# Optimization experiments

Measured on AMD Instinct MI355X. Metric: run time of the kernel, lower is better.

The kernel has to match this reference:

```python
import jax, jax.numpy as jnp
import numpy as np

B, C, H, W = 32, 3, 224, 224
PH = PW = 16
N = (H // PH) * (W // PW)          # 196 patches
PATCH_DIM = C * PH * PW             # 768
DIM = 512
NUM_CLASSES = 1000
LAMBDA = 1.0                        # lambda_=1 in OptimAttn
RHO = 1.0                           # ADMM penalty
ADMM_ITERS = 50                     # fixed iteration count (jit-friendly)
LN_EPS = 1e-5


def layernorm(x, g, b):
    mu = jnp.mean(x, axis=-1, keepdims=True)
    var = jnp.mean((x - mu) ** 2, axis=-1, keepdims=True)
    return (x - mu) / jnp.sqrt(var + LN_EPS) * g + b


def box_qp_admm(Q1, p, iters=ADMM_ITERS, rho=RHO):
    """Solve min_x 0.5 x^T Q1 x + p^T x  s.t. 0 <= x <= 1, batched.
    Q1: [b, m, m] (shared across the n query tokens), p: [b, n, m].
    ADMM splitting x = z; x-update uses the precomputed inverse of (Q1 + rho I).
    Returns z: [b, n, m] (feasible iterate)."""
    b, n, m = p.shape
    Minv = jnp.linalg.inv(Q1 + rho * jnp.eye(m, dtype=Q1.dtype))  # [b, m, m]

    def step(carry, _):
        z, u = carry
        rhs = rho * (z - u) - p                        # [b, n, m]
        x = jnp.einsum('bij,bnj->bni', Minv, rhs)       # [b, n, m]
        z = jnp.clip(x + u, 0.0, 1.0)                   # box projection (lb=0, ub=1)
        u = u + x - z
        return (z, u), None

    z0 = jnp.zeros_like(p)
    u0 = jnp.zeros_like(p)
    (z, _), _ = jax.lax.scan(step, (z0, u0), None, length=iters)
    return z


def setup_inputs() -> dict:
    key = jax.random.key(0)
    ks = jax.random.split(key, 8)
    s = 0.02
    return {
        'img': jax.random.normal(ks[0], (B, C, H, W), jnp.float32),
        'ln_patch_g': jnp.ones((PATCH_DIM,), jnp.float32),
        'ln_patch_b': jnp.zeros((PATCH_DIM,), jnp.float32),
        'wq_w': jax.random.normal(ks[1], (PATCH_DIM, DIM), jnp.float32) * s,
        'wq_b': jnp.zeros((DIM,), jnp.float32),
        'lnq_g': jnp.ones((DIM,), jnp.float32),
        'lnq_b': jnp.zeros((DIM,), jnp.float32),
        'wv_w': jax.random.normal(ks[2], (PATCH_DIM, DIM), jnp.float32) * s,
        'wv_b': jnp.zeros((DIM,), jnp.float32),
        'lnv_g': jnp.ones((DIM,), jnp.float32),
        'lnv_b': jnp.zeros((DIM,), jnp.float32),
        'pos_emb': jax.random.normal(ks[3], (1, N + 1, PATCH_DIM), jnp.float32),
        'mlp_ln_g': jnp.ones((DIM,), jnp.float32),
        'mlp_ln_b': jnp.zeros((DIM,), jnp.float32),
        'mlp_w': jax.random.normal(ks[4], (DIM, NUM_CLASSES), jnp.float32) * s,
        'mlp_b': jnp.zeros((NUM_CLASSES,), jnp.float32),
    }


def reference(img, ln_patch_g, ln_patch_b, wq_w, wq_b, lnq_g, lnq_b,
              wv_w, wv_b, lnv_g, lnv_b, pos_emb, mlp_ln_g, mlp_ln_b,
              mlp_w, mlp_b):
    b = img.shape[0]
    # patchify: b c (h ph) (w pw) -> b (h w) (c ph pw)
    hh, ww = H // PH, W // PW
    x = img.reshape(b, C, hh, PH, ww, PW).transpose(0, 2, 4, 1, 3, 5)
    x = x.reshape(b, hh * ww, PATCH_DIM)
    x = layernorm(x, ln_patch_g, ln_patch_b)
    n = x.shape[1]
    x = x + pos_emb[:, :n]

    Q = layernorm(x @ wq_w + wq_b, lnq_g, lnq_b)   # [b, n, d]
    V = layernorm(x @ wv_w + wv_b, lnv_g, lnv_b)   # [b, m, d]

    # Attention via per-token box QP
    m = V.shape[1]
    V = V / m
    Q1 = 2.0 * jnp.einsum('bmd,bkd->bmk', V, V)                 # [b, m, m]
    p = -2.0 * jnp.einsum('bmd,bnd->bnm', V, Q) + LAMBDA / m    # [b, n, m]
    z = box_qp_admm(Q1, p)                                      # [b, n, m]

    coeffs = z / (jnp.sum(jnp.abs(z), axis=-1, keepdims=True) + 1e-10)
    out = jnp.einsum('bnm,bmd->bnd', coeffs, V)                 # [b, n, d]

    pooled = out.mean(axis=1)                                   # [b, d]
    logits = layernorm(pooled, mlp_ln_g, mlp_ln_b) @ mlp_w + mlp_b
    return jax.nn.softmax(logits, axis=-1)
```

## Files before the change

kernel.cpp:

```cpp
#include <hip/hip_runtime.h>

#define B_ 32
#define NP 196
#define PD 768
#define DM 512
#define NC 1000
#define MAT (NP*NP)

typedef __attribute__((ext_vector_type(8))) short short8;
typedef __attribute__((ext_vector_type(16))) float f32x16;
typedef __attribute__((ext_vector_type(2))) float f32x2;

__device__ inline unsigned short f2bf(float x) {
  union { float f; unsigned u; } c; c.f = x;
  unsigned r = c.u + 0x7FFFu + ((c.u >> 16) & 1u);
  return (unsigned short)(r >> 16);
}
__device__ inline float bf2f(unsigned short h) {
  union { unsigned u; float f; } c; c.u = ((unsigned)h) << 16; return c.f;
}

__device__ inline void pack_store_hi(unsigned short* Bh, int base,
                                     float r0, float r1, float r2, float r3) {
  unsigned short h0=f2bf(r0), h1=f2bf(r1), h2=f2bf(r2), h3=f2bf(r3);
  uint2 vh; vh.x = (unsigned)h0 | ((unsigned)h1<<16); vh.y = (unsigned)h2 | ((unsigned)h3<<16);
  *reinterpret_cast<uint2*>(Bh + base) = vh;
}

__global__ __launch_bounds__(256) void k_patchify(
    const float* __restrict__ img, const float* __restrict__ g,
    const float* __restrict__ be, const float* __restrict__ pos,
    unsigned short* __restrict__ Xh) {
  int bn = blockIdx.x;
  int b = bn / NP, n = bn % NP;
  int gh = n / 14, gw = n % 14;
  int t = threadIdx.x;
  float vals[3]; float s = 0.f, ss = 0.f;
  #pragma unroll
  for (int k = 0; k < 3; ++k) {
    int e = t + (k << 8);
    int inner = e & 255;
    int ph = inner >> 4, pw = inner & 15;
    float v = img[((b*3 + k)*224 + gh*16 + ph)*224 + gw*16 + pw];
    vals[k] = v; s += v; ss += v*v;
  }
  __shared__ float rb[8];
  for (int o = 32; o; o >>= 1) { s += __shfl_down(s,o); ss += __shfl_down(ss,o); }
  if ((t & 63) == 0) { rb[t>>6] = s; rb[4+(t>>6)] = ss; }
  __syncthreads();
  float S = rb[0]+rb[1]+rb[2]+rb[3], SS = rb[4]+rb[5]+rb[6]+rb[7];
  float mu = S * (1.f/768.f);
  float var = SS * (1.f/768.f) - mu*mu;
  float inv = rsqrtf(var + 1e-5f);
  int mt = bn >> 5, ml = bn & 31;
  size_t base = (size_t)mt * 48 * 512;
  #pragma unroll
  for (int k = 0; k < 3; ++k) {
    int e = t + (k << 8);
    float val = (vals[k]-mu)*inv*g[e] + be[e] + pos[n*PD + e];
    int ks = e >> 4, h = (e >> 3) & 1, j = e & 7;
    size_t idx = base + ((size_t)ks*64 + ml + 32*h)*8 + j;
    Xh[idx] = f2bf(val);
  }
}

__global__ __launch_bounds__(256) void k_wswz(
    const float* __restrict__ W,
    unsigned short* __restrict__ Bh) {
  int k = blockIdx.x;
  int t = threadIdx.x;
  int ks = k >> 4, h = (k >> 3) & 1, j = k & 7;
  #pragma unroll
  for (int q = 0; q < 2; ++q) {
    int n = t + (q << 8);
    float v = W[(size_t)k*512 + n];
    size_t idx = (((size_t)(n>>5)*48 + ks)*64 + (n&31) + 32*h)*8 + j;
    Bh[idx] = f2bf(v);
  }
}

__global__ __launch_bounds__(256, 1) void k_qv_mfma(
    const unsigned short* __restrict__ Xh,
    const unsigned short* __restrict__ Wqh,
    const unsigned short* __restrict__ Wvh,
    const float* __restrict__ bq, const float* __restrict__ bv,
    float* __restrict__ qo, float* __restrict__ vo) {
  int bid = blockIdx.x;
  int proj = bid & 1, nq = (bid >> 1) & 3, mp = bid >> 3;
  int mt0 = mp*2, mt1 = mp*2 + 1;
  const unsigned short* Bh = proj ? Wvh : Wqh;
  const float* bias = proj ? bv : bq;
  float* out = proj ? vo : qo;
  int t = threadIdx.x, wv = t >> 6, l = t & 63;
  int n_l = l & 31, h = l >> 5;
  int nt = nq*4 + wv;
  const unsigned short* a0h_p = Xh + (size_t)mt0*48*512 + l*8;
  const unsigned short* a1h_p = Xh + (size_t)mt1*48*512 + l*8;
  const unsigned short* bh_p = Bh + (size_t)nt*48*512 + l*8;
  f32x16 p1_0, p1_1;
  #pragma unroll
  for (int i = 0; i < 16; ++i) { p1_0[i]=0.f; p1_1[i]=0.f; }
  #pragma unroll 4
  for (int ks = 0; ks < 48; ++ks) {
    short8 bh = *reinterpret_cast<const short8*>(bh_p + (size_t)ks*512);
    short8 a0h = *reinterpret_cast<const short8*>(a0h_p + (size_t)ks*512);
    short8 a1h = *reinterpret_cast<const short8*>(a1h_p + (size_t)ks*512);
    p1_0 = __builtin_amdgcn_mfma_f32_32x32x16_bf16(a0h, bh, p1_0, 0, 0, 0);
    p1_1 = __builtin_amdgcn_mfma_f32_32x32x16_bf16(a1h, bh, p1_1, 0, 0, 0);
  }
  float bb = bias[nt*32 + n_l];
  #pragma unroll
  for (int r = 0; r < 16; ++r) {
    int rl = (r&3) + 8*(r>>2) + 4*h;
    out[(size_t)(mt0*32 + rl)*512 + nt*32 + n_l] = p1_0[r] + bb;
    out[(size_t)(mt1*32 + rl)*512 + nt*32 + n_l] = p1_1[r] + bb;
  }
}

__global__ __launch_bounds__(256) void k_ln2(
    const float* __restrict__ q, float* __restrict__ v,
    const float* __restrict__ gq, const float* __restrict__ bq,
    const float* __restrict__ gv, const float* __restrict__ bv,
    unsigned short* __restrict__ Fh) {
  int r = blockIdx.x; bool hv = (r >= B_*NP); if (hv) r -= B_*NP;
  const float* X = hv ? v : q;
  const float* g  = hv ? gv : gq;
  const float* be = hv ? bv : bq;
  float scale = hv ? (1.f/196.f) : 1.f;
  int t = threadIdx.x;
  float v0 = X[(size_t)r*512 + t], v1 = X[(size_t)r*512 + 256 + t];
  float s = v0+v1, ss = v0*v0+v1*v1;
  __shared__ float rb[8];
  for (int o = 32; o; o >>= 1) { s += __shfl_down(s,o); ss += __shfl_down(ss,o); }
  if ((t&63)==0) { rb[t>>6]=s; rb[4+(t>>6)]=ss; }
  __syncthreads();
  float S = rb[0]+rb[1]+rb[2]+rb[3], SS = rb[4]+rb[5]+rb[6]+rb[7];
  float mu = S*(1.f/512.f), var = SS*(1.f/512.f)-mu*mu;
  float inv = rsqrtf(var+1e-5f);
  int b = r / NP, ntok = r % NP;
  int mt = ntok >> 5, ml = ntok & 31;
  size_t fb = (((size_t)b*2 + (hv?1:0))*7 + mt) * 32 * 512;
  float val0 = ((v0-mu)*inv*g[t]+be[t])*scale;
  float val1 = ((v1-mu)*inv*g[t+256]+be[t+256])*scale;
  if (hv) {
    v[(size_t)r*512+t] = val0;
    v[(size_t)r*512+256+t] = val1;
  }
  #pragma unroll
  for (int e2 = 0; e2 < 2; ++e2) {
    int e = t + (e2 << 8);
    float val = e2 ? val1 : val0;
    int ks = e >> 4, h = (e >> 3) & 1, j = e & 7;
    size_t idx = fb + (size_t)ks*512 + ((size_t)ml + 32*h)*8 + j;
    Fh[idx] = f2bf(val);
  }
}

__global__ __launch_bounds__(64) void k_gram_mfma(
    const unsigned short* __restrict__ Fh,
    float* __restrict__ Ao, float* __restrict__ po) {
  int gid = blockIdx.x;
  int mt = gid / 7, nt = gid % 7;
  int z = blockIdx.y; int b = z & 31; bool hp = (z >= 32);
  int l = threadIdx.x;
  int col = l & 31, h2 = l >> 5;
  size_t abase = (((size_t)b*2 + (hp ? 0 : 1))*7 + mt) * 32 * 512 + l*8;
  size_t bbase = (((size_t)b*2 + 1)*7 + nt) * 32 * 512 + l*8;
  f32x16 a1;
  #pragma unroll
  for (int i = 0; i < 16; ++i) { a1[i] = 0.f; }
  #pragma unroll 4
  for (int ks = 0; ks < 32; ++ks) {
    short8 ah = *reinterpret_cast<const short8*>(Fh + abase + (size_t)ks*512);
    short8 bh = *reinterpret_cast<const short8*>(Fh + bbase + (size_t)ks*512);
    a1 = __builtin_amdgcn_mfma_f32_32x32x16_bf16(ah, bh, a1, 0, 0, 0);
  }
  float alpha  = hp ? -2.f : 2.f;
  float diagAdd = hp ? 0.f : 1.f;
  float cAdd   = hp ? (1.f/196.f) : 0.f;
  float* out = (hp ? po : Ao) + (size_t)b*MAT;
  #pragma unroll
  for (int r = 0; r < 16; ++r) {
    int m = mt*32 + (r&3) + 8*(r>>2) + 4*h2;
    int c = nt*32 + col;
    if (m < NP && c < NP)
      out[(size_t)m*NP + c] = alpha*a1[r] + cAdd + (m==c ? diagAdd : 0.f);
  }
}

__global__ __launch_bounds__(256) void k_nsinit2(
    const float* __restrict__ A, float* __restrict__ X, float* __restrict__ Y) {
  int b = blockIdx.x, t = threadIdx.x;
  const float* Ab = A + (size_t)b*MAT;
  __shared__ float sm[256];
  float lm = 0.f;
  if (t < NP) {
    float s = 0.f;
    for (int j = 0; j < NP; ++j) {
      float v = Ab[t*NP + j];
      if (j == t) v -= 1.f;
      s += fabsf(v);
    }
    lm = s;
  }
  sm[t] = lm; __syncthreads();
  for (int o = 128; o; o >>= 1) { if (t < o) sm[t] = fmaxf(sm[t], sm[t+o]); __syncthreads(); }
  float cc = 2.f / (2.f + sm[0]);
  float* Xb = X + (size_t)b*MAT;
  float* Yb = Y + (size_t)b*MAT;
  for (int idx = t; idx < MAT; idx += 256) {
    float yv = cc * Ab[idx];
    Yb[idx] = yv;
    float tpr = cc * yv;
    Xb[idx] = ((idx % (NP+1) == 0) ? 2.f*cc : 0.f) - tpr;
  }
}

__global__ __launch_bounds__(256) void k_ns(
    const float* __restrict__ X, const float* __restrict__ Y,
    float* __restrict__ Xn, float* __restrict__ Yn) {
  int zz = blockIdx.z; int b = zz & 31; bool hy = (zz >= 32);
  const float* Lb = (hy ? Y : X) + (size_t)b*MAT;
  const float* Rb = Y + (size_t)b*MAT;
  float* Ob = (hy ? Yn : Xn) + (size_t)b*MAT;
  int c0 = blockIdx.x * 64, r0 = blockIdx.y * 64;
  __shared__ __align__(16) float Ls[16][68];
  __shared__ __align__(16) float Rs[16][64];
  int t = threadIdx.x, tx = t & 15, ty = t >> 4;
  int alr = t >> 2, alc = (t & 3) << 2;
  int blr = t >> 4, blc = (t & 15) << 2;
  f32x2 acc[4][2];
  #pragma unroll
  for (int i = 0; i < 4; ++i) { acc[i][0] = 0.f; acc[i][1] = 0.f; }
  int lrow = min(r0 + alr, NP-1);
  for (int k0 = 0; k0 < NP; k0 += 16) {
    float4 lv = {0.f,0.f,0.f,0.f};
    if (k0 + alc < NP) lv = *reinterpret_cast<const float4*>(&Lb[(size_t)lrow*NP + k0 + alc]);
    float4 rv = {0.f,0.f,0.f,0.f};
    if (k0 + blr < NP) rv = *reinterpret_cast<const float4*>(&Rb[(size_t)(k0+blr)*NP + c0 + blc]);
    Ls[alc+0][alr] = lv.x; Ls[alc+1][alr] = lv.y;
    Ls[alc+2][alr] = lv.z; Ls[alc+3][alr] = lv.w;
    *reinterpret_cast<float4*>(&Rs[blr][blc]) = rv;
    __syncthreads();
    #pragma unroll
    for (int kt = 0; kt < 16; ++kt) {
      float a4[4];
      *reinterpret_cast<float4*>(a4) = *reinterpret_cast<const float4*>(&Ls[kt][ty<<2]);
      const f32x2* b2 = reinterpret_cast<const f32x2*>(&Rs[kt][tx<<2]);
      f32x2 b20 = b2[0], b21 = b2[1];
      #pragma unroll
      for (int i = 0; i < 4; ++i) {
        f32x2 av; av[0] = a4[i]; av[1] = a4[i];
        acc[i][0] += av * b20;
        acc[i][1] += av * b21;
      }
    }
    __syncthreads();
  }
  #pragma unroll
  for (int i = 0; i < 4; ++i) {
    int r = r0 + (ty<<2) + i; if (r >= NP) continue;
    #pragma unroll
    for (int j = 0; j < 4; ++j) {
      int c = c0 + (tx<<2) + j; if (c >= NP) continue;
      Ob[(size_t)r*NP + c] = 2.f*Lb[(size_t)r*NP + c] - acc[i][j>>1][j&1];
    }
  }
}

__global__ __launch_bounds__(256) void k_ns_last(
    const float* __restrict__ X, const float* __restrict__ Y,
    unsigned short* __restrict__ Ahi) {
  int b = blockIdx.z;
  const float* Lb = X + (size_t)b*MAT;
  const float* Rb = Y + (size_t)b*MAT;
  int c0 = blockIdx.x * 64, r0 = blockIdx.y * 64;
  __shared__ __align__(16) float Ls[16][68];
  __shared__ __align__(16) float Rs[16][64];
  int t = threadIdx.x, tx = t & 15, ty = t >> 4;
  int alr = t >> 2, alc = (t & 3) << 2;
  int blr = t >> 4, blc = (t & 15) << 2;
  f32x2 acc[4][2];
  #pragma unroll
  for (int i = 0; i < 4; ++i) { acc[i][0] = 0.f; acc[i][1] = 0.f; }
  int lrow = min(r0 + alr, NP-1);
  for (int k0 = 0; k0 < NP; k0 += 16) {
    float4 lv = {0.f,0.f,0.f,0.f};
    if (k0 + alc < NP) lv = *reinterpret_cast<const float4*>(&Lb[(size_t)lrow*NP + k0 + alc]);
    float4 rv = {0.f,0.f,0.f,0.f};
    if (k0 + blr < NP) rv = *reinterpret_cast<const float4*>(&Rb[(size_t)(k0+blr)*NP + c0 + blc]);
    Ls[alc+0][alr] = lv.x; Ls[alc+1][alr] = lv.y;
    Ls[alc+2][alr] = lv.z; Ls[alc+3][alr] = lv.w;
    *reinterpret_cast<float4*>(&Rs[blr][blc]) = rv;
    __syncthreads();
    #pragma unroll
    for (int kt = 0; kt < 16; ++kt) {
      float a4[4];
      *reinterpret_cast<float4*>(a4) = *reinterpret_cast<const float4*>(&Ls[kt][ty<<2]);
      const f32x2* b2 = reinterpret_cast<const f32x2*>(&Rs[kt][tx<<2]);
      f32x2 b20 = b2[0], b21 = b2[1];
      #pragma unroll
      for (int i = 0; i < 4; ++i) {
        f32x2 av; av[0] = a4[i]; av[1] = a4[i];
        acc[i][0] += av * b20;
        acc[i][1] += av * b21;
      }
    }
    __syncthreads();
  }
  #pragma unroll
  for (int i = 0; i < 4; ++i) {
    int r = r0 + (ty<<2) + i; if (r >= NP) continue;
    #pragma unroll
    for (int j = 0; j < 4; ++j) {
      int c = c0 + (tx<<2) + j; if (c >= NP) continue;
      float val = 2.f*Lb[(size_t)r*NP + c] - acc[i][j>>1][j&1];
      size_t idx = (((size_t)(b*7 + (r>>5))*13) + (c>>4))*512
                 + (size_t)((r&31) + 32*((c>>3)&1))*8 + (c&7);
      Ahi[idx] = f2bf(val);
    }
  }
}

__global__ __launch_bounds__(448) void k_admm7(
    const unsigned short* __restrict__ Ahi,
    const float* __restrict__ P, float* __restrict__ w) {
  int bid = blockIdx.x;
  int b = bid & 31, tt = bid >> 5;
  int t = threadIdx.x;
  int wv = t >> 6;
  int l = t & 63;
  int n_l = l & 31, h = l >> 5;
  int n = tt*32 + n_l;
  int mt = wv;

  __shared__ __align__(16) unsigned short Bhi[2][14*512];
  __shared__ float ssum[7][32];

  float z[16], u[16], pr[16];
  int ngc = min(n, NP-1);
  const float* prow = P + ((size_t)b*NP + ngc)*NP;
  #pragma unroll
  for (int r = 0; r < 16; ++r) {
    int m = mt*32 + (r&3) + 8*(r>>2) + 4*h;
    pr[r] = prow[min(m, NP-1)];
    z[r] = 0.f; u[r] = 0.f;
  }
  #pragma unroll
  for (int g = 0; g < 4; ++g) {
    int base_ = ((mt*4 + g)*32 + n_l)*8 + 4*h;
    pack_store_hi(&Bhi[0][0], base_,
                  -pr[4*g], -pr[4*g+1], -pr[4*g+2], -pr[4*g+3]);
  }

  const unsigned short* ah_g = Ahi + ((size_t)(b*7 + mt)*13)*512 + l*8;
  short8 Amh[13];
  #pragma unroll
  for (int ks = 0; ks < 13; ++ks) {
    Amh[ks] = *reinterpret_cast<const short8*>(ah_g + (size_t)ks*512);
  }
  int boff = (h*32 + n_l)*8;
  __syncthreads();

  for (int it = 0; it < 50; ++it) {
    int rb_ = it & 1, wb_ = rb_ ^ 1;
    const unsigned short* bh_s = &Bhi[rb_][boff];
    f32x16 acc1;
    #pragma unroll
    for (int i = 0; i < 16; ++i) { acc1[i] = 0.f; }
    #pragma unroll
    for (int ks = 0; ks < 13; ++ks) {
      short8 bh = *reinterpret_cast<const short8*>(bh_s + ks*512);
      acc1 = __builtin_amdgcn_mfma_f32_32x32x16_bf16(Amh[ks], bh, acc1, 0, 0, 0);
    }
    #pragma unroll
    for (int g = 0; g < 4; ++g) {
      float rr[4];
      #pragma unroll
      for (int j = 0; j < 4; ++j) {
        int r = 4*g + j;
        float xpu = acc1[r] + u[r];
        float zz = fminf(fmaxf(xpu, 0.f), 1.f);
        u[r] = xpu - zz;
        z[r] = zz;
        rr[j] = zz - u[r] - pr[r];
      }
      int base_ = ((mt*4 + g)*32 + n_l)*8 + 4*h;
      pack_store_hi(&Bhi[wb_][0], base_, rr[0], rr[1], rr[2], rr[3]);
    }
    __syncthreads();
  }

  float s = 0.f;
  #pragma unroll
  for (int r = 0; r < 16; ++r) {
    int m = mt*32 + (r&3) + 8*(r>>2) + 4*h;
    if (m < NP) s += z[r];
  }
  s += __shfl_xor(s, 32, 64);
  if (l < 32) ssum[wv][n_l] = s;
  __syncthreads();
  float stot = 0.f;
  #pragma unroll
  for (int q = 0; q < 7; ++q) stot += ssum[q][n_l];
  float inv = (n < NP) ? 1.f/(stot + 1e-10f) : 0.f;
  #pragma unroll
  for (int r = 0; r < 16; ++r) {
    float c = z[r] * inv * (1.f/196.f);
    #pragma unroll
    for (int o = 16; o; o >>= 1) c += __shfl_xor(c, o, 64);
    if (n_l == 0) {
      int m = mt*32 + (r&3) + 8*(r>>2) + 4*h;
      if (m < NP) atomicAdd(&w[b*NP + m], c);
    }
  }
}

__global__ __launch_bounds__(256) void k_pool(
    const float* __restrict__ w, const float* __restrict__ V,
    const float* __restrict__ g, const float* __restrict__ be,
    float* __restrict__ pl_g) {
  int b = blockIdx.x, t = threadIdx.x;
  __shared__ float ws_[NP];
  __shared__ float rb[8];
  if (t < NP) ws_[t] = w[b*NP + t];
  __syncthreads();
  const float* Vb = V + (size_t)b*NP*512;
  float a0 = 0.f, a1 = 0.f;
  #pragma unroll 4
  for (int m = 0; m < NP; ++m) {
    float wm = ws_[m];
    a0 = fmaf(wm, Vb[(size_t)m*512 + t], a0);
    a1 = fmaf(wm, Vb[(size_t)m*512 + 256 + t], a1);
  }
  float s = a0+a1, ss = a0*a0+a1*a1;
  for (int o = 32; o; o >>= 1) { s += __shfl_down(s,o); ss += __shfl_down(ss,o); }
  if ((t&63)==0) { rb[t>>6]=s; rb[4+(t>>6)]=ss; }
  __syncthreads();
  float S = rb[0]+rb[1]+rb[2]+rb[3], SS = rb[4]+rb[5]+rb[6]+rb[7];
  float mu = S*(1.f/512.f), var = SS*(1.f/512.f)-mu*mu, inv = rsqrtf(var+1e-5f);
  pl_g[(size_t)b*512 + t]       = (a0-mu)*inv*g[t] + be[t];
  pl_g[(size_t)b*512 + 256 + t] = (a1-mu)*inv*g[t+256] + be[t+256];
}

__global__ __launch_bounds__(512) void k_head(
    const float* __restrict__ pl_g, const float* __restrict__ Wm,
    const float* __restrict__ bm, float* __restrict__ logits) {
  int cg = blockIdx.x, b = blockIdx.y;
  int t = threadIdx.x;
  int c0 = cg * 125;
  __shared__ float pl[512];
  __shared__ float part[4][128];
  pl[t] = pl_g[(size_t)b*512 + t];
  __syncthreads();
  int kk = t >> 7, cc = t & 127;
  float a = 0.f;
  if (cc < 125) {
    int c = c0 + cc;
    const float* wp = Wm + (size_t)(kk*128)*NC + c;
    #pragma unroll 8
    for (int k = 0; k < 128; ++k) a = fmaf(pl[kk*128 + k], wp[(size_t)k*NC], a);
  }
  part[kk][cc] = a;
  __syncthreads();
  if (t < 125) {
    float lg = part[0][t] + part[1][t] + part[2][t] + part[3][t] + bm[c0 + t];
    logits[(size_t)b*NC + c0 + t] = lg;
  }
}

__global__ __launch_bounds__(256) void k_soft(
    const float* __restrict__ logits, float* __restrict__ out) {
  int b = blockIdx.x, t = threadIdx.x;
  __shared__ float rb[8];
  float lg[4];
  #pragma unroll
  for (int q = 0; q < 4; ++q) {
    int c = t + (q<<8);
    lg[q] = (c < NC) ? logits[(size_t)b*NC + c] : -1e30f;
  }
  float mx = fmaxf(fmaxf(lg[0],lg[1]), fmaxf(lg[2],lg[3]));
  for (int o = 32; o; o >>= 1) mx = fmaxf(mx, __shfl_down(mx,o));
  if ((t&63)==0) rb[t>>6] = mx;
  __syncthreads();
  float MX = fmaxf(fmaxf(rb[0],rb[1]), fmaxf(rb[2],rb[3]));
  float es = 0.f, ev[4];
  #pragma unroll
  for (int q = 0; q < 4; ++q) {
    int c = t + (q<<8);
    ev[q] = (c < NC) ? __expf(lg[q]-MX) : 0.f;
    es += ev[q];
  }
  for (int o = 32; o; o >>= 1) es += __shfl_down(es,o);
  __syncthreads();
  if ((t&63)==0) rb[4+(t>>6)] = es;
  __syncthreads();
  float SUM = rb[4]+rb[5]+rb[6]+rb[7];
  float rinv = 1.f/SUM;
  #pragma unroll
  for (int q = 0; q < 4; ++q) {
    int c = t + (q<<8);
    if (c < NC) out[(size_t)b*NC + c] = ev[q]*rinv;
  }
}

extern "C" void kernel_launch(void* const* d_in, const int* in_sizes, int n_in,
                              void* d_out, int out_size, void* d_ws, size_t ws_size,
                              hipStream_t stream) {
  const float* img = (const float*)d_in[0];
  const float* lpg = (const float*)d_in[1];
  const float* lpb = (const float*)d_in[2];
  const float* wqw = (const float*)d_in[3];
  const float* wqb = (const float*)d_in[4];
  const float* lqg = (const float*)d_in[5];
  const float* lqb = (const float*)d_in[6];
  const float* wvw = (const float*)d_in[7];
  const float* wvb = (const float*)d_in[8];
  const float* lvg = (const float*)d_in[9];
  const float* lvb = (const float*)d_in[10];
  const float* pos = (const float*)d_in[11];
  const float* mlg = (const float*)d_in[12];
  const float* mlb = (const float*)d_in[13];
  const float* mw  = (const float*)d_in[14];
  const float* mb  = (const float*)d_in[15];
  float* outp = (float*)d_out;

  float* ws = (float*)d_ws;
  size_t off = 0;
  float* q  = ws + off;      off += (size_t)B_*NP*DM;
  float* v  = ws + off;      off += (size_t)B_*NP*DM;
  size_t matp = (size_t)B_*MAT + 256;
  float* A  = ws + off;      off += matp;
  float* p  = ws + off;      off += matp;
  float* Xa = ws + off;      off += matp;
  float* Xb = ws + off;      off += matp;
  float* Ya = ws + off;      off += matp;
  float* Yb = A;
  float* w  = ws + off;      off += (size_t)B_*NP;
  float* pl_g = ws + off;    off += (size_t)B_*DM;
  float* logits = ws + off;  off += (size_t)B_*NC;
  off = (off + 3) & ~(size_t)3;
  size_t swzE = (size_t)B_*7*13*512;
  unsigned short* Ahi = (unsigned short*)(ws + off); off += swzE/2;
  unsigned short* Alo = (unsigned short*)(ws + off); off += swzE/2;
  size_t xfE = (size_t)196*48*512;
  unsigned short* Xfh = (unsigned short*)(ws + off); off += xfE/2;
  unsigned short* Xfl = (unsigned short*)(ws + off); off += xfE/2;
  size_t wfE = (size_t)16*48*512;
  unsigned short* Wqh = (unsigned short*)(ws + off); off += wfE/2;
  unsigned short* Wql = (unsigned short*)(ws + off); off += wfE/2;
  unsigned short* Wvh = (unsigned short*)(ws + off); off += wfE/2;
  unsigned short* Wvl = (unsigned short*)(ws + off); off += wfE/2;
  size_t qvfE = (size_t)B_*2*7*32*512;
  unsigned short* Fh = (unsigned short*)(ws + off); off += qvfE/2;
  unsigned short* Fl = (unsigned short*)(ws + off); off += qvfE/2;
  if (ws_size < off * sizeof(float)) return;
  (void)Alo; (void)Xfl; (void)Wql; (void)Wvl; (void)Fl;

  k_wswz<<<dim3(768), 256, 0, stream>>>(wqw, Wqh);
  k_wswz<<<dim3(768), 256, 0, stream>>>(wvw, Wvh);
  k_patchify<<<dim3(B_*NP), 256, 0, stream>>>(img, lpg, lpb, pos, Xfh);
  k_qv_mfma<<<dim3(784), 256, 0, stream>>>(Xfh, Wqh, Wvh, wqb, wvb, q, v);
  k_ln2<<<dim3(2*B_*NP), 256, 0, stream>>>(q, v, lqg, lqb, lvg, lvb, Fh);
  k_gram_mfma<<<dim3(49, 64), 64, 0, stream>>>(Fh, A, p);
  (void)hipMemsetAsync(Ahi, 0, swzE * sizeof(unsigned short), stream);
  k_nsinit2<<<dim3(B_), 256, 0, stream>>>(A, Xa, Ya);
  k_ns<<<dim3(4,4,32), 256, 0, stream>>>(Ya, Ya, Yb, Yb);
  k_ns<<<dim3(4,4,64), 256, 0, stream>>>(Xa, Yb, Xb, Ya);
  k_ns_last<<<dim3(4,4,32), 256, 0, stream>>>(Xb, Ya, Ahi);
  (void)hipMemsetAsync(w, 0, (size_t)B_*NP*sizeof(float), stream);
  k_admm7<<<dim3(7*B_), 448, 0, stream>>>(Ahi, p, w);
  k_pool<<<dim3(B_), 256, 0, stream>>>(w, v, mlg, mlb, pl_g);
  k_head<<<dim3(8, B_), 512, 0, stream>>>(pl_g, mw, mb, logits);
  k_soft<<<dim3(B_), 256, 0, stream>>>(logits, outp);
}
```

Baseline: 355.2 us.

## Merge weight swizzle launches, parallelize NS init, split ADMM MFMA accumulator chain

Three unrelated changes. The two weight-swizzle kernels are merged into one launch. The Newton-Schulz init kernel now computes row sums with one wave per row plus shuffle reductions and vectorized float4 stores, where before each thread serially scanned a whole row. The 50-iteration ADMM inner loop splits its 13 dependent MFMAs into two independent accumulator chains to shorten the dependency latency. The cost is extra accumulator registers in the ADMM kernel.

```diff
diff --git a/kernel.cpp b/kernel.cpp
--- a/kernel.cpp
+++ b/kernel.cpp
@@ -64,10 +64,14 @@
   }
 }
 
-__global__ __launch_bounds__(256) void k_wswz(
-    const float* __restrict__ W,
-    unsigned short* __restrict__ Bh) {
-  int k = blockIdx.x;
+__global__ __launch_bounds__(256) void k_wswz2(
+    const float* __restrict__ Wq, const float* __restrict__ Wv,
+    unsigned short* __restrict__ Qh, unsigned short* __restrict__ Vh) {
+  int bid = blockIdx.x;
+  bool pv = (bid >= 768);
+  int k = pv ? bid - 768 : bid;
+  const float* W = pv ? Wv : Wq;
+  unsigned short* Bh = pv ? Vh : Qh;
   int t = threadIdx.x;
   int ks = k >> 4, h = (k >> 3) & 1, j = k & 7;
   #pragma unroll
@@ -192,27 +196,40 @@
     const float* __restrict__ A, float* __restrict__ X, float* __restrict__ Y) {
   int b = blockIdx.x, t = threadIdx.x;
   const float* Ab = A + (size_t)b*MAT;
-  __shared__ float sm[256];
-  float lm = 0.f;
-  if (t < NP) {
+  __shared__ float rowsum[NP];
+  __shared__ float redbuf[4];
+  int wv = t >> 6, l = t & 63;
+  for (int r = wv; r < NP; r += 4) {
     float s = 0.f;
-    for (int j = 0; j < NP; ++j) {
-      float v = Ab[t*NP + j];
-      if (j == t) v -= 1.f;
-      s += fabsf(v);
-    }
-    lm = s;
-  }
-  sm[t] = lm; __syncthreads();
-  for (int o = 128; o; o >>= 1) { if (t < o) sm[t] = fmaxf(sm[t], sm[t+o]); __syncthreads(); }
-  float cc = 2.f / (2.f + sm[0]);
-  float* Xb = X + (size_t)b*MAT;
-  float* Yb = Y + (size_t)b*MAT;
-  for (int idx = t; idx < MAT; idx += 256) {
-    float yv = cc * Ab[idx];
-    Yb[idx] = yv;
-    float tpr = cc * yv;
-    Xb[idx] = ((idx % (NP+1) == 0) ? 2.f*cc : 0.f) - tpr;
+    for (int c = l; c < NP; c += 64) {
+      float vv = Ab[(size_t)r*NP + c];
+      if (c == r) vv -= 1.f;
+      s += fabsf(vv);
+    }
+    for (int o = 32; o; o >>= 1) s += __shfl_down(s, o);
+    if (l == 0) rowsum[r] = s;
+  }
+  __syncthreads();
+  float lm = (t < NP) ? rowsum[t] : 0.f;
+  for (int o = 32; o; o >>= 1) lm = fmaxf(lm, __shfl_down(lm, o));
+  if ((t & 63) == 0) redbuf[t>>6] = lm;
+  __syncthreads();
+  float mx = fmaxf(fmaxf(redbuf[0], redbuf[1]), fmaxf(redbuf[2], redbuf[3]));
+  float cc = 2.f / (2.f + mx);
+  const float4* A4 = reinterpret_cast<const float4*>(Ab);
+  float4* X4 = reinterpret_cast<float4*>(X + (size_t)b*MAT);
+  float4* Y4 = reinterpret_cast<float4*>(Y + (size_t)b*MAT);
+  for (int i = t; i < MAT/4; i += 256) {
+    float4 av = A4[i];
+    float4 yv = {cc*av.x, cc*av.y, cc*av.z, cc*av.w};
+    int base = i*4;
+    float4 xv;
+    #pragma unroll
+    for (int k = 0; k < 4; ++k) {
+      float tpr = cc * (&yv.x)[k];
+      (&xv.x)[k] = (((base + k) % (NP+1) == 0) ? 2.f*cc : 0.f) - tpr;
+    }
+    X4[i] = xv; Y4[i] = yv;
   }
 }
 
@@ -365,13 +382,19 @@
   for (int it = 0; it < 50; ++it) {
     int rb_ = it & 1, wb_ = rb_ ^ 1;
     const unsigned short* bh_s = &Bhi[rb_][boff];
-    f32x16 acc1;
-    #pragma unroll
-    for (int i = 0; i < 16; ++i) { acc1[i] = 0.f; }
-    #pragma unroll
-    for (int ks = 0; ks < 13; ++ks) {
-      short8 bh = *reinterpret_cast<const short8*>(bh_s + ks*512);
-      acc1 = __builtin_amdgcn_mfma_f32_32x32x16_bf16(Amh[ks], bh, acc1, 0, 0, 0);
+    f32x16 acc_a, acc_b;
+    #pragma unroll
+    for (int i = 0; i < 16; ++i) { acc_a[i] = 0.f; acc_b[i] = 0.f; }
+    #pragma unroll
+    for (int ks = 0; ks < 6; ++ks) {
+      short8 bha = *reinterpret_cast<const short8*>(bh_s + (2*ks)*512);
+      short8 bhb = *reinterpret_cast<const short8*>(bh_s + (2*ks+1)*512);
+      acc_a = __builtin_amdgcn_mfma_f32_32x32x16_bf16(Amh[2*ks],   bha, acc_a, 0, 0, 0);
+      acc_b = __builtin_amdgcn_mfma_f32_32x32x16_bf16(Amh[2*ks+1], bhb, acc_b, 0, 0, 0);
+    }
+    {
+      short8 bha = *reinterpret_cast<const short8*>(bh_s + 12*512);
+      acc_a = __builtin_amdgcn_mfma_f32_32x32x16_bf16(Amh[12], bha, acc_a, 0, 0, 0);
     }
     #pragma unroll
     for (int g = 0; g < 4; ++g) {
@@ -379,7 +402,7 @@
       #pragma unroll
       for (int j = 0; j < 4; ++j) {
         int r = 4*g + j;
-        float xpu = acc1[r] + u[r];
+        float xpu = acc_a[r] + acc_b[r] + u[r];
         float zz = fminf(fmaxf(xpu, 0.f), 1.f);
         u[r] = xpu - zz;
         z[r] = zz;
@@ -557,8 +580,7 @@
   if (ws_size < off * sizeof(float)) return;
   (void)Alo; (void)Xfl; (void)Wql; (void)Wvl; (void)Fl;
 
-  k_wswz<<<dim3(768), 256, 0, stream>>>(wqw, Wqh);
-  k_wswz<<<dim3(768), 256, 0, stream>>>(wvw, Wvh);
+  k_wswz2<<<dim3(1536), 256, 0, stream>>>(wqw, wvw, Wqh, Wvh);
   k_patchify<<<dim3(B_*NP), 256, 0, stream>>>(img, lpg, lpb, pos, Xfh);
   k_qv_mfma<<<dim3(784), 256, 0, stream>>>(Xfh, Wqh, Wvh, wqb, wvb, q, v);
   k_ln2<<<dim3(2*B_*NP), 256, 0, stream>>>(q, v, lqg, lqb, lvg, lvb, Fh);
```

Result: slower. 393.5 us (+10.8%).
